# Optimization experiments

Hardware: AMD Instinct MI355X
Metric: run time of the kernel (lower is better)

Reference implementation:

```python
import jax, jax.numpy as jnp
import numpy as np

ALPHA_SCALE = 9.9
EPS_LN = 1e-5
EPS_NORM = 1e-12


def _ln(x, g, b):
    m = x.mean(axis=-1, keepdims=True)
    v = ((x - m) ** 2).mean(axis=-1, keepdims=True)
    return (x - m) / jnp.sqrt(v + EPS_LN) * g + b


def setup_inputs() -> dict:
    key = jax.random.key(0)
    ks = jax.random.split(key, 8)
    B, D, U = 32, 4096, 64
    return {
        "stimulus": jax.random.normal(ks[0], (B, D), jnp.float32),
        "prev_act": jax.random.normal(ks[1], (B, D), jnp.float32),
        "W_heb": jax.random.normal(ks[2], (D, D), jnp.float32),
        "W_rec": jax.random.normal(ks[3], (D, D), jnp.float32),
        "decay": jax.random.uniform(ks[4], (D,), jnp.float32),
        "ln_rec_g": jnp.ones((D,), jnp.float32),
        "ln_rec_b": jnp.zeros((D,), jnp.float32),
        "fc1_w": jax.random.normal(ks[5], (D, 512), jnp.float32) * 0.02,
        "fc1_b": jnp.zeros((512,), jnp.float32),
        "ln1_g": jnp.ones((512,), jnp.float32),
        "ln1_b": jnp.zeros((512,), jnp.float32),
        "fc2_w": jax.random.normal(ks[6], (512, 256), jnp.float32) * 0.05,
        "fc2_b": jnp.zeros((256,), jnp.float32),
        "ln2_g": jnp.ones((256,), jnp.float32),
        "ln2_b": jnp.zeros((256,), jnp.float32),
        "fc3_w": jax.random.normal(ks[7], (256, U), jnp.float32) * 0.05,
        "fc3_b": jnp.zeros((U,), jnp.float32),
        "lno_g": jnp.ones((U,), jnp.float32),
        "lno_b": jnp.zeros((U,), jnp.float32),
    }


def reference(stimulus, prev_act, W_heb, W_rec, decay, ln_rec_g, ln_rec_b,
              fc1_w, fc1_b, ln1_g, ln1_b, fc2_w, fc2_b, ln2_g, ln2_b,
              fc3_w, fc3_b, lno_g, lno_b):
    D = W_heb.shape[0]
    U = fc3_b.shape[0]
    # recurrent path
    rec_out = jax.nn.relu(prev_act @ W_rec)           # [B, D]
    rec_norm = _ln(rec_out, ln_rec_g, ln_rec_b)
    # stimulus path
    stim_out = jax.nn.relu(stimulus @ W_heb)          # [B, D]
    final = stim_out + rec_norm                       # [B, D]
    # neuromodulator MLP -> dopamine (mean over batch)
    h = jax.nn.relu(_ln(final @ fc1_w + fc1_b, ln1_g, ln1_b))
    h = jax.nn.relu(_ln(h @ fc2_w + fc2_b, ln2_g, ln2_b))
    dop = jnp.tanh(_ln(h @ fc3_w + fc3_b, lno_g, lno_b)).mean(axis=0)  # [U]
    alpha = jnp.repeat(dop, D // U) * ALPHA_SCALE                      # [D]
    # Hebbian updates: batched outer products accumulated = GEMM
    heb_upd = jnp.einsum('bi,bj->ij', stimulus, stim_out)   # [D, D]
    rec_upd = jnp.einsum('bi,bj->ij', prev_act, rec_out)    # [D, D]
    W1 = W_heb + heb_upd * alpha[None, :]
    W2 = W_rec + rec_upd * alpha[None, :]
    # decay: W - diag(decay) @ W == (1 - decay) row-scale
    W1 = W1 * (1.0 - decay)[:, None]
    W2 = W2 * (1.0 - decay)[:, None]
    # row-wise L2 normalize (F.normalize p=2 dim=1)
    W1 = W1 / jnp.maximum(jnp.linalg.norm(W1, axis=1, keepdims=True), EPS_NORM)
    W2 = W2 / jnp.maximum(jnp.linalg.norm(W2, axis=1, keepdims=True), EPS_NORM)
    # [B+2D, D]: final_output followed by the two updated weight buffers
    return jnp.concatenate([final, W1, W2], axis=0)
```

## Files before the change

### kernel.cpp

```cpp
#include <hip/hip_runtime.h>
#include <stdint.h>

typedef unsigned short ushort_t;
typedef float f32x4 __attribute__((ext_vector_type(4)));
typedef short s16x8 __attribute__((ext_vector_type(8)));

#define B_  32
#define D_  4096
#define H1_ 512
#define H2_ 256
#define U_  64

#define KS_   16
#define KCH_  256
#define NT_   128
#define APAD  264
#define WPAD  72

__device__ __forceinline__ float bf2f(ushort_t u) {
    return __uint_as_float(((uint32_t)u) << 16);
}
__device__ __forceinline__ ushort_t f2bfu(float f) {
    uint32_t x = __float_as_uint(f);
    return (ushort_t)((x + 0x7fffu + ((x >> 16) & 1u)) >> 16);
}
__device__ __forceinline__ uint32_t pk2bf(float a, float b) {
    return ((uint32_t)f2bfu(a)) | (((uint32_t)f2bfu(b)) << 16);
}

__global__ __launch_bounds__(256, 4) void k_gemm_mfma(
    const float* __restrict__ stim, const float* __restrict__ prev,
    const float* __restrict__ Wheb, const float* __restrict__ Wrec,
    float* __restrict__ Psum, int ns)
{
    __shared__ ushort_t Al[32 * APAD];
    __shared__ ushort_t Wt[NT_ * WPAD];

    int bx = blockIdx.x;
    int gemm  = bx >> 9;
    int rem   = bx & 511;
    int nblk  = rem >> 4;
    int chunk = rem & 15;
    const float* A = gemm ? prev : stim;
    const float* W = gemm ? Wrec : Wheb;
    int k0c = chunk * KCH_;
    int n0  = nblk * NT_;
    int tid = threadIdx.x, lane = tid & 63, wave = tid >> 6;
    int col = lane & 15, quad = lane >> 4;

#pragma unroll
    for (int p = 0; p < 16; p++) {
        int idx = p * 256 + tid;
        int b   = idx >> 7;
        int kk  = (idx & 127) * 2;
        float2 v = *(const float2*)(A + (size_t)b * D_ + k0c + kk);
        *(uint32_t*)&Al[b * APAD + kk] = pk2bf(v.x, v.y);
    }

    f32x4 acc[2][2];
#pragma unroll
    for (int mt = 0; mt < 2; mt++)
#pragma unroll
        for (int nt = 0; nt < 2; nt++)
            acc[mt][nt] = (f32x4){0.f, 0.f, 0.f, 0.f};

    int wcol = tid & 127;
    int kh   = (tid >> 7) * 32;

    for (int ks = 0; ks < 4; ks++) {
        __syncthreads();
        const float* Wc = W + (size_t)(k0c + ks * 64 + kh) * D_ + n0 + wcol;
        uint32_t* dst = (uint32_t*)&Wt[wcol * WPAD] + (kh >> 1);
#pragma unroll
        for (int i = 0; i < 16; i++) {
            float a = Wc[(size_t)(2 * i) * D_];
            float b = Wc[(size_t)(2 * i + 1) * D_];
            dst[i] = pk2bf(a, b);
        }
        __syncthreads();

#pragma unroll
        for (int kq = 0; kq < 2; kq++) {
            int kb = ks * 64 + kq * 32 + quad * 8;
            int kw = kq * 32 + quad * 8;
            s16x8 af[2], bf[2];
            af[0] = *(const s16x8*)&Al[col * APAD + kb];
            af[1] = *(const s16x8*)&Al[(col + 16) * APAD + kb];
#pragma unroll
            for (int nt = 0; nt < 2; nt++)
                bf[nt] = *(const s16x8*)&Wt[(wave * 32 + nt * 16 + col) * WPAD + kw];
#pragma unroll
            for (int mt = 0; mt < 2; mt++)
#pragma unroll
                for (int nt = 0; nt < 2; nt++)
                    acc[mt][nt] = __builtin_amdgcn_mfma_f32_16x16x32_bf16(
                        af[mt], bf[nt], acc[mt][nt], 0, 0, 0);
        }
    }

    int slice = chunk % ns;
    float* P = Psum + ((size_t)slice * 2 + gemm) * 32 * D_;
    if (ns == 16) {
#pragma unroll
        for (int mt = 0; mt < 2; mt++)
#pragma unroll
            for (int nt = 0; nt < 2; nt++)
#pragma unroll
                for (int r = 0; r < 4; r++) {
                    int b = mt * 16 + quad * 4 + r;
                    int n = n0 + wave * 32 + nt * 16 + col;
                    P[(size_t)b * D_ + n] = acc[mt][nt][r];
                }
    } else {
#pragma unroll
        for (int mt = 0; mt < 2; mt++)
#pragma unroll
            for (int nt = 0; nt < 2; nt++)
#pragma unroll
                for (int r = 0; r < 4; r++) {
                    int b = mt * 16 + quad * 4 + r;
                    int n = n0 + wave * 32 + nt * 16 + col;
                    atomicAdd(&P[(size_t)b * D_ + n], acc[mt][nt][r]);
                }
    }
}

__global__ __launch_bounds__(256) void k_reduce(
    const float* __restrict__ Psum,
    const float* __restrict__ stim, const float* __restrict__ prev,
    float* __restrict__ P_relu, ushort_t* __restrict__ Tbuf, int ns)
{
    int idx = blockIdx.x * 256 + threadIdx.x;
    int gemm = idx >> 17;
    int r    = idx & 131071;
    int b    = r >> 12;
    int d    = r & 4095;
    float s = 0.f;
    for (int sl = 0; sl < ns; sl++)
        s += Psum[((size_t)sl * 2 + gemm) * 131072 + r];
    s = fmaxf(s, 0.f);
    P_relu[idx] = s;
    Tbuf[(2 + gemm) * 131072 + d * 32 + b] = f2bfu(s);
    Tbuf[gemm * 131072 + d * 32 + b] = f2bfu((gemm ? prev : stim)[r]);
}

__global__ __launch_bounds__(256) void k_final_ln(
    const float* __restrict__ P_relu,
    const float* __restrict__ g, const float* __restrict__ be,
    float* __restrict__ dout, float* __restrict__ finalf32)
{
    __shared__ float red[256], red2[256];
    int b = blockIdx.x, tid = threadIdx.x;
    const float* rec = P_relu + 131072 + b * D_;
    const float* stm = P_relu + b * D_;

    float s = 0.f, s2 = 0.f;
    for (int d = tid; d < D_; d += 256) { float x = rec[d]; s += x; s2 += x * x; }
    red[tid] = s; red2[tid] = s2; __syncthreads();
    for (int st = 128; st > 0; st >>= 1) {
        if (tid < st) { red[tid] += red[tid + st]; red2[tid] += red2[tid + st]; }
        __syncthreads();
    }
    float m = red[0] * (1.f / D_);
    float v = red2[0] * (1.f / D_) - m * m;
    float rstd = rsqrtf(v + 1e-5f);

    for (int d = tid; d < D_; d += 256) {
        float fn = stm[d] + (rec[d] - m) * rstd * g[d] + be[d];
        finalf32[b * D_ + d] = fn;
        dout[b * D_ + d] = fn;
    }
}

__global__ __launch_bounds__(256) void k_fc1(
    const float* __restrict__ finalf32, const float* __restrict__ fc1w,
    float* __restrict__ z1p)
{
    int kc = blockIdx.x;
    int t  = threadIdx.x;
    int k0 = kc * 64;
    const float2* W2 = (const float2*)fc1w;

    float a0[32], a1[32];
#pragma unroll
    for (int b = 0; b < 32; b++) { a0[b] = 0.f; a1[b] = 0.f; }

    for (int k = k0; k < k0 + 64; k++) {
        float2 wv = W2[k * (H1_ / 2) + t];
#pragma unroll
        for (int b = 0; b < 32; b++) {
            float a = finalf32[b * D_ + k];
            a0[b] = fmaf(a, wv.x, a0[b]);
            a1[b] = fmaf(a, wv.y, a1[b]);
        }
    }
    float* P = z1p + (size_t)kc * 32 * H1_;
#pragma unroll
    for (int b = 0; b < 32; b++) {
        P[b * H1_ + 2 * t]     = a0[b];
        P[b * H1_ + 2 * t + 1] = a1[b];
    }
}

__global__ __launch_bounds__(256) void k_tail(
    const float* __restrict__ z1p,
    const float* __restrict__ fc1b,
    const float* __restrict__ ln1g, const float* __restrict__ ln1b,
    const float* __restrict__ fc2w, const float* __restrict__ fc2b,
    const float* __restrict__ ln2g, const float* __restrict__ ln2b,
    const float* __restrict__ fc3w, const float* __restrict__ fc3b,
    const float* __restrict__ lnog, const float* __restrict__ lnob,
    float* __restrict__ tanhout)
{
    __shared__ float sm[512];
    __shared__ float red[256], red2[256];
    __shared__ float h2s[256];
    int b = blockIdx.x, tid = threadIdx.x;

    for (int j = tid; j < H1_; j += 256) {
        float s = fc1b[j];
        for (int c = 0; c < 64; c++)
            s += z1p[((size_t)c * 32 + b) * H1_ + j];
        sm[j] = s;
    }
    __syncthreads();

    float s = 0.f, s2 = 0.f;
    for (int j = tid; j < H1_; j += 256) { float x = sm[j]; s += x; s2 += x * x; }
    red[tid] = s; red2[tid] = s2; __syncthreads();
    for (int st = 128; st > 0; st >>= 1) {
        if (tid < st) { red[tid] += red[tid + st]; red2[tid] += red2[tid + st]; }
        __syncthreads();
    }
    float m = red[0] * (1.f / H1_);
    float v = red2[0] * (1.f / H1_) - m * m;
    float rstd = rsqrtf(v + 1e-5f);
    __syncthreads();
    for (int j = tid; j < H1_; j += 256) {
        float h = (sm[j] - m) * rstd * ln1g[j] + ln1b[j];
        sm[j] = fmaxf(h, 0.f);
    }
    __syncthreads();

    float acc = fc2b[tid];
    for (int k = 0; k < H1_; k++)
        acc = fmaf(sm[k], fc2w[k * H2_ + tid], acc);
    red[tid] = acc; red2[tid] = acc * acc; __syncthreads();
    for (int st = 128; st > 0; st >>= 1) {
        if (tid < st) { red[tid] += red[tid + st]; red2[tid] += red2[tid + st]; }
        __syncthreads();
    }
    float m2 = red[0] * (1.f / H2_);
    float v2 = red2[0] * (1.f / H2_) - m2 * m2;
    float rstd2 = rsqrtf(v2 + 1e-5f);
    float h2 = fmaxf((acc - m2) * rstd2 * ln2g[tid] + ln2b[tid], 0.f);
    __syncthreads();
    h2s[tid] = h2; __syncthreads();

    int j  = tid & 63;
    int ks = tid >> 6;
    float p = 0.f;
    for (int kk = 0; kk < 64; kk++) {
        int k = ks * 64 + kk;
        p = fmaf(h2s[k], fc3w[k * U_ + j], p);
    }
    red[tid] = p; __syncthreads();
    if (tid < 64) {
        float x = red[tid] + red[tid + 64] + red[tid + 128] + red[tid + 192]
                + fc3b[tid];
        float ss = x, qq = x * x;
#pragma unroll
        for (int off = 32; off; off >>= 1) {
            ss += __shfl_xor(ss, off, 64);
            qq += __shfl_xor(qq, off, 64);
        }
        float m3 = ss * (1.f / U_);
        float v3 = qq * (1.f / U_) - m3 * m3;
        float to = tanhf((x - m3) * rsqrtf(v3 + 1e-5f) * lnog[tid] + lnob[tid]);
        tanhout[b * U_ + tid] = to;
    }
}

__global__ __launch_bounds__(256) void k_update(
    const float* __restrict__ Wheb, const float* __restrict__ Wrec,
    const float* __restrict__ decay, const float* __restrict__ tanhout,
    const ushort_t* __restrict__ Tbuf, float* __restrict__ dout)
{
    __shared__ ushort_t cache[8 * 4096];
    int bx = blockIdx.x;
    int mat   = bx >> 9;
    int itile = bx & 511;
    int i0    = itile * 8;
    int tid  = threadIdx.x;
    int wv   = tid >> 6;
    int lane = tid & 63;
    int ir0 = i0 + wv * 2, ir1 = ir0 + 1;

    float al = 0.f;
#pragma unroll
    for (int b = 0; b < 32; b++) al += tanhout[b * U_ + lane];
    al *= (9.9f / 32.f);

    const ushort_t* Sp = Tbuf + mat * 131072;
    const uint4* s0p = (const uint4*)(Sp + (size_t)ir0 * 32);
    const uint4* s1p = (const uint4*)(Sp + (size_t)ir1 * 32);
    float st0[32], st1[32];
#pragma unroll
    for (int q = 0; q < 4; q++) {
        uint4 a = s0p[q], c = s1p[q];
        const uint32_t aw[4] = {a.x, a.y, a.z, a.w};
        const uint32_t cw[4] = {c.x, c.y, c.z, c.w};
#pragma unroll
        for (int e = 0; e < 4; e++) {
            st0[q * 8 + 2 * e]     = __uint_as_float(aw[e] << 16);
            st0[q * 8 + 2 * e + 1] = __uint_as_float(aw[e] & 0xffff0000u);
            st1[q * 8 + 2 * e]     = __uint_as_float(cw[e] << 16);
            st1[q * 8 + 2 * e + 1] = __uint_as_float(cw[e] & 0xffff0000u);
        }
    }
    float dc0 = 1.f - decay[ir0];
    float dc1 = 1.f - decay[ir1];

    const ushort_t* Op = Tbuf + (2 + mat) * 131072;
    const float* Wp = mat ? Wrec : Wheb;

    float ss0 = 0.f, ss1 = 0.f;
    for (int jt = 0; jt < 64; jt++) {
        int j = jt * 64 + lane;
        float av = __shfl(al, jt, 64);
        const uint4* op = (const uint4*)(Op + (size_t)j * 32);
        float u0 = 0.f, u1 = 0.f;
#pragma unroll
        for (int q = 0; q < 4; q++) {
            uint4 a = op[q];
            const uint32_t w4[4] = {a.x, a.y, a.z, a.w};
#pragma unroll
            for (int e = 0; e < 4; e++) {
                float o0 = __uint_as_float(w4[e] << 16);
                float o1 = __uint_as_float(w4[e] & 0xffff0000u);
                u0 = fmaf(st0[q * 8 + 2 * e], o0, u0);
                u0 = fmaf(st0[q * 8 + 2 * e + 1], o1, u0);
                u1 = fmaf(st1[q * 8 + 2 * e], o0, u1);
                u1 = fmaf(st1[q * 8 + 2 * e + 1], o1, u1);
            }
        }
        float w0v = Wp[(size_t)ir0 * D_ + j];
        float w1v = Wp[(size_t)ir1 * D_ + j];
        float v0 = (w0v + av * u0) * dc0;
        float v1 = (w1v + av * u1) * dc1;
        ss0 += v0 * v0;
        ss1 += v1 * v1;
        cache[(wv * 2) * 4096 + j]     = f2bfu(v0);
        cache[(wv * 2 + 1) * 4096 + j] = f2bfu(v1);
    }
#pragma unroll
    for (int off = 32; off; off >>= 1) {
        ss0 += __shfl_xor(ss0, off, 64);
        ss1 += __shfl_xor(ss1, off, 64);
    }
    float ri0 = 1.f / fmaxf(sqrtf(ss0), 1e-12f);
    float ri1 = 1.f / fmaxf(sqrtf(ss1), 1e-12f);

    float* O0 = dout + (size_t)(32 + mat * D_ + ir0) * D_;
    float* O1 = O0 + D_;
    for (int j = lane; j < D_; j += 64) {
        O0[j] = bf2f(cache[(wv * 2) * 4096 + j]) * ri0;
        O1[j] = bf2f(cache[(wv * 2 + 1) * 4096 + j]) * ri1;
    }
}

extern "C" void kernel_launch(void* const* d_in, const int* in_sizes, int n_in,
                              void* d_out, int out_size, void* d_ws, size_t ws_size,
                              hipStream_t stream)
{
    const float* stim = (const float*)d_in[0];
    const float* prev = (const float*)d_in[1];
    const float* Wheb = (const float*)d_in[2];
    const float* Wrec = (const float*)d_in[3];
    const float* decay= (const float*)d_in[4];
    const float* lnrg = (const float*)d_in[5];
    const float* lnrb = (const float*)d_in[6];
    const float* fc1w = (const float*)d_in[7];
    const float* fc1b = (const float*)d_in[8];
    const float* ln1g = (const float*)d_in[9];
    const float* ln1b = (const float*)d_in[10];
    const float* fc2w = (const float*)d_in[11];
    const float* fc2b = (const float*)d_in[12];
    const float* ln2g = (const float*)d_in[13];
    const float* ln2b = (const float*)d_in[14];
    const float* fc3w = (const float*)d_in[15];
    const float* fc3b = (const float*)d_in[16];
    const float* lnog = (const float*)d_in[17];
    const float* lnob = (const float*)d_in[18];

    const size_t FIXED = 1048576u + 1048576u + 524288u + 4194304u + 8192u;
    int ns = 16;
    if (ws_size < FIXED + 16u * 1048576u) {
        size_t avail = (ws_size > FIXED) ? (ws_size - FIXED) / 1048576u : 1u;
        ns = (int)avail;
        if (ns < 1) ns = 1;
        if (ns > 16) ns = 16;
    }

    char* ws = (char*)d_ws;
    float*    P_sum   = (float*)(ws + 0);
    char*     rest    = ws + (size_t)ns * 1048576u;
    float*    P_relu  = (float*)(rest + 0);
    ushort_t* P_tbuf  = (ushort_t*)(rest + 1048576);
    float*    P_final = (float*)(rest + 2097152);
    float*    P_z1p   = (float*)(rest + 2621440);
    float*    P_tanh  = (float*)(rest + 6815744);

    float* out = (float*)d_out;

    if (ns < 16)
        hipMemsetAsync(P_sum, 0, (size_t)ns * 1048576u, stream);

    k_gemm_mfma<<<1024, 256, 0, stream>>>(stim, prev, Wheb, Wrec, P_sum, ns);
    k_reduce   <<<1024, 256, 0, stream>>>(P_sum, stim, prev, P_relu, P_tbuf, ns);
    k_final_ln <<<32,   256, 0, stream>>>(P_relu, lnrg, lnrb, out, P_final);
    k_fc1      <<<64,   256, 0, stream>>>(P_final, fc1w, P_z1p);
    k_tail     <<<32,   256, 0, stream>>>(P_z1p, fc1b, ln1g, ln1b, fc2w, fc2b,
                                          ln2g, ln2b, fc3w, fc3b, lnog, lnob, P_tanh);
    k_update   <<<1024, 256, 0, stream>>>(Wheb, Wrec, decay, P_tanh, P_tbuf, out);
}
```

Measured before the change: 424.9 us.

## Rewrite Hebbian update kernel with bf16 MFMA and register-resident row cache

The outer-product accumulation in the weight-update kernel now uses a 16x16x32 bf16 MFMA per 16x16 tile instead of per-lane scalar FMA loops. Updated values are held packed as bf16 in registers rather than a 64KB LDS cache. Row sums of squares are combined across 8 waves through a small shared array. Blocks grow to 512 threads covering 16 rows each, which cuts redundant operand loads and LDS pressure but raises register use.

```diff
diff --git a/kernel.cpp b/kernel.cpp
--- a/kernel.cpp
+++ b/kernel.cpp
@@ -281,20 +281,18 @@
     }
 }
 
-__global__ __launch_bounds__(256) void k_update(
+__global__ __launch_bounds__(512, 2) void k_update(
     const float* __restrict__ Wheb, const float* __restrict__ Wrec,
     const float* __restrict__ decay, const float* __restrict__ tanhout,
     const ushort_t* __restrict__ Tbuf, float* __restrict__ dout)
 {
-    __shared__ ushort_t cache[8 * 4096];
-    int bx = blockIdx.x;
-    int mat   = bx >> 9;
-    int itile = bx & 511;
-    int i0    = itile * 8;
+    __shared__ float ssl[8][16];
+    int bx   = blockIdx.x;
+    int mat  = bx >> 8;
+    int i0   = (bx & 255) * 16;
     int tid  = threadIdx.x;
-    int wv   = tid >> 6;
-    int lane = tid & 63;
-    int ir0 = i0 + wv * 2, ir1 = ir0 + 1;
+    int wave = tid >> 6, lane = tid & 63;
+    int col  = lane & 15, quad = lane >> 4;
 
     float al = 0.f;
 #pragma unroll
@@ -302,70 +300,69 @@
     al *= (9.9f / 32.f);
 
     const ushort_t* Sp = Tbuf + mat * 131072;
-    const uint4* s0p = (const uint4*)(Sp + (size_t)ir0 * 32);
-    const uint4* s1p = (const uint4*)(Sp + (size_t)ir1 * 32);
-    float st0[32], st1[32];
-#pragma unroll
-    for (int q = 0; q < 4; q++) {
-        uint4 a = s0p[q], c = s1p[q];
-        const uint32_t aw[4] = {a.x, a.y, a.z, a.w};
-        const uint32_t cw[4] = {c.x, c.y, c.z, c.w};
-#pragma unroll
-        for (int e = 0; e < 4; e++) {
-            st0[q * 8 + 2 * e]     = __uint_as_float(aw[e] << 16);
-            st0[q * 8 + 2 * e + 1] = __uint_as_float(aw[e] & 0xffff0000u);
-            st1[q * 8 + 2 * e]     = __uint_as_float(cw[e] << 16);
-            st1[q * 8 + 2 * e + 1] = __uint_as_float(cw[e] & 0xffff0000u);
-        }
-    }
-    float dc0 = 1.f - decay[ir0];
-    float dc1 = 1.f - decay[ir1];
-
     const ushort_t* Op = Tbuf + (2 + mat) * 131072;
-    const float* Wp = mat ? Wrec : Wheb;
-
-    float ss0 = 0.f, ss1 = 0.f;
-    for (int jt = 0; jt < 64; jt++) {
-        int j = jt * 64 + lane;
-        float av = __shfl(al, jt, 64);
-        const uint4* op = (const uint4*)(Op + (size_t)j * 32);
-        float u0 = 0.f, u1 = 0.f;
-#pragma unroll
-        for (int q = 0; q < 4; q++) {
-            uint4 a = op[q];
-            const uint32_t w4[4] = {a.x, a.y, a.z, a.w};
-#pragma unroll
-            for (int e = 0; e < 4; e++) {
-                float o0 = __uint_as_float(w4[e] << 16);
-                float o1 = __uint_as_float(w4[e] & 0xffff0000u);
-                u0 = fmaf(st0[q * 8 + 2 * e], o0, u0);
-                u0 = fmaf(st0[q * 8 + 2 * e + 1], o1, u0);
-                u1 = fmaf(st1[q * 8 + 2 * e], o0, u1);
-                u1 = fmaf(st1[q * 8 + 2 * e + 1], o1, u1);
-            }
-        }
-        float w0v = Wp[(size_t)ir0 * D_ + j];
-        float w1v = Wp[(size_t)ir1 * D_ + j];
-        float v0 = (w0v + av * u0) * dc0;
-        float v1 = (w1v + av * u1) * dc1;
-        ss0 += v0 * v0;
-        ss1 += v1 * v1;
-        cache[(wv * 2) * 4096 + j]     = f2bfu(v0);
-        cache[(wv * 2 + 1) * 4096 + j] = f2bfu(v1);
-    }
-#pragma unroll
-    for (int off = 32; off; off >>= 1) {
-        ss0 += __shfl_xor(ss0, off, 64);
-        ss1 += __shfl_xor(ss1, off, 64);
-    }
-    float ri0 = 1.f / fmaxf(sqrtf(ss0), 1e-12f);
-    float ri1 = 1.f / fmaxf(sqrtf(ss1), 1e-12f);
-
-    float* O0 = dout + (size_t)(32 + mat * D_ + ir0) * D_;
-    float* O1 = O0 + D_;
-    for (int j = lane; j < D_; j += 64) {
-        O0[j] = bf2f(cache[(wv * 2) * 4096 + j]) * ri0;
-        O1[j] = bf2f(cache[(wv * 2 + 1) * 4096 + j]) * ri1;
+    const float*    Wp = mat ? Wrec : Wheb;
+
+    s16x8 af = *(const s16x8*)&Sp[(i0 + col) * 32 + quad * 8];
+
+    float dc[4];
+#pragma unroll
+    for (int r = 0; r < 4; r++) dc[r] = 1.f - decay[i0 + quad * 4 + r];
+
+    uint32_t vc[32][2];
+    float ss[4] = {0.f, 0.f, 0.f, 0.f};
+
+#pragma unroll
+    for (int t = 0; t < 32; t++) {
+        int j0 = (t * 8 + wave) * 16;
+        float av = __shfl(al, j0 >> 6, 64);
+        s16x8 bfr = *(const s16x8*)&Op[(j0 + col) * 32 + quad * 8];
+        f32x4 u = (f32x4){0.f, 0.f, 0.f, 0.f};
+        u = __builtin_amdgcn_mfma_f32_16x16x32_bf16(af, bfr, u, 0, 0, 0);
+        const float* wrow = Wp + (size_t)(i0 + quad * 4) * D_ + j0 + col;
+        float v0 = fmaf(av, u[0], wrow[0])              * dc[0];
+        float v1 = fmaf(av, u[1], wrow[(size_t)1 * D_]) * dc[1];
+        float v2 = fmaf(av, u[2], wrow[(size_t)2 * D_]) * dc[2];
+        float v3 = fmaf(av, u[3], wrow[(size_t)3 * D_]) * dc[3];
+        ss[0] = fmaf(v0, v0, ss[0]);
+        ss[1] = fmaf(v1, v1, ss[1]);
+        ss[2] = fmaf(v2, v2, ss[2]);
+        ss[3] = fmaf(v3, v3, ss[3]);
+        vc[t][0] = pk2bf(v0, v1);
+        vc[t][1] = pk2bf(v2, v3);
+    }
+
+#pragma unroll
+    for (int off = 8; off; off >>= 1) {
+#pragma unroll
+        for (int r = 0; r < 4; r++) ss[r] += __shfl_xor(ss[r], off, 64);
+    }
+    if (col == 0) {
+#pragma unroll
+        for (int r = 0; r < 4; r++) ssl[wave][quad * 4 + r] = ss[r];
+    }
+    __syncthreads();
+    float ri[4];
+#pragma unroll
+    for (int r = 0; r < 4; r++) {
+        float s = 0.f;
+#pragma unroll
+        for (int w = 0; w < 8; w++) s += ssl[w][quad * 4 + r];
+        ri[r] = 1.f / fmaxf(sqrtf(s), 1e-12f);
+    }
+
+    float* O = dout + (size_t)(32 + mat * D_ + i0 + quad * 4) * D_;
+#pragma unroll
+    for (int t = 0; t < 32; t++) {
+        int j0 = (t * 8 + wave) * 16;
+        float v0 = __uint_as_float(vc[t][0] << 16);
+        float v1 = __uint_as_float(vc[t][0] & 0xffff0000u);
+        float v2 = __uint_as_float(vc[t][1] << 16);
+        float v3 = __uint_as_float(vc[t][1] & 0xffff0000u);
+        O[j0 + col]                   = v0 * ri[0];
+        O[(size_t)1 * D_ + j0 + col]  = v1 * ri[1];
+        O[(size_t)2 * D_ + j0 + col]  = v2 * ri[2];
+        O[(size_t)3 * D_ + j0 + col]  = v3 * ri[3];
     }
 }
 
@@ -422,5 +419,5 @@
     k_fc1      <<<64,   256, 0, stream>>>(P_final, fc1w, P_z1p);
     k_tail     <<<32,   256, 0, stream>>>(P_z1p, fc1b, ln1g, ln1b, fc2w, fc2b,
                                           ln2g, ln2b, fc3w, fc3b, lnog, lnob, P_tanh);
-    k_update   <<<1024, 256, 0, stream>>>(Wheb, Wrec, decay, P_tanh, P_tbuf, out);
-}
+    k_update   <<<512,  512, 0, stream>>>(Wheb, Wrec, decay, P_tanh, P_tbuf, out);
+}
```

New measurement: 409.4 us. 3.7% less time.
